# Performance work log

Hardware: AMD Instinct MI355X
Metric: run time of the kernel (lower is better)

## Reference

```python
import jax, jax.numpy as jnp
import numpy as np

B, S, D, H = 2, 2048, 1024, 16
DK = D // H


def setup_inputs() -> dict:
    key = jax.random.key(0)
    ks = jax.random.split(key, 8)
    scale = 1.0 / np.sqrt(D)
    inp = {
        "query": jax.random.normal(ks[0], (B, S, D), dtype=jnp.float32),
        "key": jax.random.normal(ks[1], (B, S, D), dtype=jnp.float32),
        "value": jax.random.normal(ks[2], (B, S, D), dtype=jnp.float32),
        # causal mask, broadcastable over batch and heads
        "mask": jnp.tril(jnp.ones((S, S), dtype=jnp.int32))[None, None, :, :],
        "W_q": jax.random.normal(ks[3], (D, D), dtype=jnp.float32) * scale,
        "W_k": jax.random.normal(ks[4], (D, D), dtype=jnp.float32) * scale,
        "W_v": jax.random.normal(ks[5], (D, D), dtype=jnp.float32) * scale,
        "W_o": jax.random.normal(ks[6], (D, D), dtype=jnp.float32) * scale,
    }
    return inp


def _split_heads(t):
    Bb, Ss, _ = t.shape
    return t.reshape(Bb, Ss, H, DK).transpose(0, 2, 1, 3)  # [B,H,S,DK]


def reference(query, key, value, mask, W_q, W_k, W_v, W_o):
    # Linear(d,d,bias=False): y = x @ W^T (torch stores weight as [out,in])
    Q = _split_heads(query @ W_q.T)
    K = _split_heads(key @ W_k.T)
    V = _split_heads(value @ W_v.T)
    scores = jnp.einsum("bhqd,bhkd->bhqk", Q, K) / jnp.sqrt(jnp.float32(DK))
    scores = jnp.where(mask == 0, -jnp.inf, scores)
    weights = jax.nn.softmax(scores, axis=-1)
    weights = jnp.nan_to_num(weights, nan=0.0)  # fully-masked rows -> 0
    # dropout is identity at inference
    x = jnp.einsum("bhqk,bhkd->bhqd", weights, V)
    x = x.transpose(0, 2, 1, 3).reshape(B, S, D)
    return x @ W_o.T
```

## Files before the change

### kernel.cpp

```cpp
#include <hip/hip_runtime.h>
#include <hip/hip_bf16.h>

#define D_MODEL 1024
#define NHEAD   16
#define HDK     64
#define SEQ     2048
#define BATCH   2
#define BS      (BATCH * SEQ)

typedef __attribute__((ext_vector_type(8))) short bf16x8;
typedef __attribute__((ext_vector_type(4))) float f32x4;

__device__ __forceinline__ unsigned short f2bf(float f) {
    unsigned u = __builtin_bit_cast(unsigned, f);
    u += 0x7fffu + ((u >> 16) & 1u);
    return (unsigned short)(u >> 16);
}

__device__ __forceinline__ unsigned pack_hi(float x, float y) {
    return __builtin_amdgcn_perm(__builtin_bit_cast(unsigned, y),
                                 __builtin_bit_cast(unsigned, x), 0x07060302u);
}

typedef const void __attribute__((address_space(1))) gas_void;
typedef void __attribute__((address_space(3))) las_void;

__device__ __forceinline__ void gll16(const void* g, void* l) {
    __builtin_amdgcn_global_load_lds((gas_void*)g, (las_void*)l, 16, 0, 0);
}

__device__ __forceinline__ void cast_body(const float* __restrict__ src,
                                          unsigned short* __restrict__ dst, int i) {
    const float4* p = (const float4*)src + (size_t)i * 2;
    float4 a = p[0], b = p[1];
    ushort4 lo = make_ushort4(f2bf(a.x), f2bf(a.y), f2bf(a.z), f2bf(a.w));
    ushort4 hi = make_ushort4(f2bf(b.x), f2bf(b.y), f2bf(b.z), f2bf(b.w));
    ushort4* q = (ushort4*)dst + (size_t)i * 2;
    q[0] = lo; q[1] = hi;
}

__global__ __launch_bounds__(256)
void cast_act(const float* a, const float* b, const float* c,
              unsigned short* oa, unsigned short* ob, unsigned short* oc, int n8) {
    int i = blockIdx.x * 256 + threadIdx.x;
    if (i >= n8) return;
    const float* s = blockIdx.y == 0 ? a : blockIdx.y == 1 ? b : c;
    unsigned short* d = blockIdx.y == 0 ? oa : blockIdx.y == 1 ? ob : oc;
    cast_body(s, d, i);
}

__global__ __launch_bounds__(256)
void cast_wt(const float* a, const float* b, const float* c, const float* dd,
             unsigned short* oa, unsigned short* ob, unsigned short* oc, unsigned short* od, int n8) {
    int i = blockIdx.x * 256 + threadIdx.x;
    if (i >= n8) return;
    const float* s = blockIdx.y == 0 ? a : blockIdx.y == 1 ? b : blockIdx.y == 2 ? c : dd;
    unsigned short* d = blockIdx.y == 0 ? oa : blockIdx.y == 1 ? ob : blockIdx.y == 2 ? oc : od;
    cast_body(s, d, i);
}

__device__ __forceinline__ void gemm_kloop128(const unsigned short* __restrict__ X,
                                              const unsigned short* __restrict__ W,
                                              unsigned short* As, unsigned short* Bs,
                                              int bm, int bn, f32x4 acc[4][4]) {
    const int t    = threadIdx.x;
    const int w    = t >> 6;
    const int L    = t & 63;
    const int quad = L >> 4;
    const int lm   = L & 15;
    const int r8   = L >> 3;
    const int sl   = L & 7;
    const int xcol = ((sl ^ r8) & 7) * 8;
    const int wr   = (w >> 1) * 64;
    const int wc   = (w & 1) * 64;

    for (int kt = 0; kt < D_MODEL; kt += 64) {
        __syncthreads();
        #pragma unroll
        for (int i = 0; i < 4; ++i) {
            int c = w * 4 + i;
            gll16(X + (size_t)(bm + c * 8 + r8) * D_MODEL + kt + xcol, &As[c * 512]);
        }
        #pragma unroll
        for (int i = 0; i < 4; ++i) {
            int c = w * 4 + i;
            gll16(W + (size_t)(bn + c * 8 + r8) * D_MODEL + kt + xcol, &Bs[c * 512]);
        }
        __syncthreads();

        #pragma unroll
        for (int ch = 0; ch < 2; ++ch) {
            bf16x8 af[4], bfr[4];
            #pragma unroll
            for (int ms = 0; ms < 4; ++ms) {
                int row = wr + ms * 16 + lm;
                af[ms] = *(const bf16x8*)&As[row * 64 + (((ch * 4 + quad) ^ (row & 7)) * 8)];
            }
            #pragma unroll
            for (int ns = 0; ns < 4; ++ns) {
                int row = wc + ns * 16 + lm;
                bfr[ns] = *(const bf16x8*)&Bs[row * 64 + (((ch * 4 + quad) ^ (row & 7)) * 8)];
            }
            #pragma unroll
            for (int ms = 0; ms < 4; ++ms)
                #pragma unroll
                for (int ns = 0; ns < 4; ++ns)
                    acc[ms][ns] = __builtin_amdgcn_mfma_f32_16x16x32_bf16(
                        af[ms], bfr[ns], acc[ms][ns], 0, 0, 0);
        }
    }
}

__device__ __forceinline__ void gemm_kloop64(const unsigned short* __restrict__ X,
                                             const unsigned short* __restrict__ W,
                                             unsigned short* As, unsigned short* Bs,
                                             int bm, int bn, f32x4 acc[2][4]) {
    const int t    = threadIdx.x;
    const int w    = t >> 6;
    const int L    = t & 63;
    const int quad = L >> 4;
    const int lm   = L & 15;
    const int r8   = L >> 3;
    const int sl   = L & 7;
    const int xcol = ((sl ^ r8) & 7) * 8;

    for (int kt = 0; kt < D_MODEL; kt += 64) {
        __syncthreads();
        #pragma unroll
        for (int i = 0; i < 4; ++i) {
            int c = w * 4 + i;
            gll16(X + (size_t)(bm + c * 8 + r8) * D_MODEL + kt + xcol, &As[c * 512]);
        }
        #pragma unroll
        for (int i = 0; i < 2; ++i) {
            int c = w * 2 + i;
            gll16(W + (size_t)(bn + c * 8 + r8) * D_MODEL + kt + xcol, &Bs[c * 512]);
        }
        __syncthreads();

        #pragma unroll
        for (int ch = 0; ch < 2; ++ch) {
            bf16x8 af[2], bfr[4];
            #pragma unroll
            for (int ms = 0; ms < 2; ++ms) {
                int row = w * 32 + ms * 16 + lm;
                af[ms] = *(const bf16x8*)&As[row * 64 + (((ch * 4 + quad) ^ (row & 7)) * 8)];
            }
            #pragma unroll
            for (int ns = 0; ns < 4; ++ns) {
                int row = ns * 16 + lm;
                bfr[ns] = *(const bf16x8*)&Bs[row * 64 + (((ch * 4 + quad) ^ (row & 7)) * 8)];
            }
            #pragma unroll
            for (int ms = 0; ms < 2; ++ms)
                #pragma unroll
                for (int ns = 0; ns < 4; ++ns)
                    acc[ms][ns] = __builtin_amdgcn_mfma_f32_16x16x32_bf16(
                        af[ms], bfr[ns], acc[ms][ns], 0, 0, 0);
        }
    }
}

__global__ __launch_bounds__(256, 3)
void proj_gemm(const unsigned short* __restrict__ qx, const unsigned short* __restrict__ kx,
               const unsigned short* __restrict__ vx, const unsigned short* __restrict__ wq,
               const unsigned short* __restrict__ wk, const unsigned short* __restrict__ wv,
               unsigned short* __restrict__ Qp, unsigned short* __restrict__ Kp,
               unsigned short* __restrict__ VT) {
    __shared__ __align__(16) unsigned short As[128 * 64];
    __shared__ __align__(16) unsigned short Bs[128 * 64];

    const int p = blockIdx.z;
    const unsigned short* X = p == 0 ? qx : p == 1 ? kx : vx;
    const unsigned short* W = p == 0 ? wq : p == 1 ? wk : wv;
    const int bm = blockIdx.y * 128, bn = blockIdx.x * 128;

    f32x4 acc[4][4];
    #pragma unroll
    for (int ms = 0; ms < 4; ++ms)
        #pragma unroll
        for (int ns = 0; ns < 4; ++ns)
            acc[ms][ns] = (f32x4){0.f, 0.f, 0.f, 0.f};

    gemm_kloop128(X, W, As, Bs, bm, bn, acc);

    const int t = threadIdx.x, w = t >> 6, L = t & 63, quad = L >> 4, lm = L & 15;
    const int wr = (w >> 1) * 64, wc = (w & 1) * 64;
    if (p == 2) {
        const int b    = bm >> 11;
        const int s_in = (bm & (SEQ - 1)) + wr;
        #pragma unroll
        for (int ms = 0; ms < 4; ++ms)
            #pragma unroll
            for (int ns = 0; ns < 4; ++ns) {
                int dg = bn + wc + ns * 16 + lm;
                int h  = dg >> 6, d = dg & 63;
                ushort4 pk = make_ushort4(f2bf(acc[ms][ns][0]), f2bf(acc[ms][ns][1]),
                                          f2bf(acc[ms][ns][2]), f2bf(acc[ms][ns][3]));
                *(ushort4*)&VT[((size_t)((b * NHEAD + h) * HDK + d)) * SEQ +
                               s_in + ms * 16 + quad * 4] = pk;
            }
    } else {
        unsigned short* Y = p == 0 ? Qp : Kp;
        const float scl = p == 0 ? 0.125f : 1.0f;
        #pragma unroll
        for (int ms = 0; ms < 4; ++ms)
            #pragma unroll
            for (int ns = 0; ns < 4; ++ns)
                #pragma unroll
                for (int r = 0; r < 4; ++r)
                    Y[(size_t)(bm + wr + ms * 16 + quad * 4 + r) * D_MODEL +
                      bn + wc + ns * 16 + lm] = f2bf(acc[ms][ns][r] * scl);
    }
}

__global__ __launch_bounds__(256)
void out_gemm(const unsigned short* __restrict__ X, const unsigned short* __restrict__ W,
              float* __restrict__ Y) {
    __shared__ __align__(16) unsigned short As[128 * 64];
    __shared__ __align__(16) unsigned short Bs[64 * 64];
    const int bm = blockIdx.y * 128, bn = blockIdx.x * 64;

    f32x4 acc[2][4];
    #pragma unroll
    for (int ms = 0; ms < 2; ++ms)
        #pragma unroll
        for (int ns = 0; ns < 4; ++ns)
            acc[ms][ns] = (f32x4){0.f, 0.f, 0.f, 0.f};

    gemm_kloop64(X, W, As, Bs, bm, bn, acc);

    const int t = threadIdx.x, w = t >> 6, L = t & 63, quad = L >> 4, lm = L & 15;
    #pragma unroll
    for (int ms = 0; ms < 2; ++ms)
        #pragma unroll
        for (int ns = 0; ns < 4; ++ns)
            #pragma unroll
            for (int r = 0; r < 4; ++r)
                Y[(size_t)(bm + w * 32 + ms * 16 + quad * 4 + r) * D_MODEL +
                  bn + ns * 16 + lm] = acc[ms][ns][r];
}

__global__ __launch_bounds__(256, 3)
void attn_mfma(const unsigned short* __restrict__ Q, const unsigned short* __restrict__ K,
               const unsigned short* __restrict__ VT, unsigned short* __restrict__ A) {
    __shared__ __align__(16) unsigned short Ks[2][64 * 72];
    __shared__ __align__(16) unsigned short Vs[2][64 * 72];
    __shared__ __align__(16) unsigned short Ps[4 * 16 * 72];

    const int t    = threadIdx.x;
    const int w    = t >> 6;
    const int L    = t & 63;
    const int quad = L >> 4;
    const int lm   = L & 15;
    const int h    = blockIdx.y;
    const int b    = blockIdx.z;
    const size_t hb  = (size_t)b * SEQ * D_MODEL + h * HDK;
    const size_t vhb = (size_t)(b * NHEAD + h) * HDK;

    const int srow = t >> 2;
    const int sc   = (t & 3) * 16;
    const unsigned short* kp = K + hb + (size_t)srow * D_MODEL + sc;
    const unsigned short* vp = VT + (vhb + srow) * SEQ + sc;
    unsigned short* ps = &Ps[w * 16 * 72];

    for (int half = 0; half < 2; ++half) {
        const int qt   = half ? 31 - (int)blockIdx.x : (int)blockIdx.x;
        const int q0   = qt * 64;
        const int qrow = q0 + w * 16 + lm;

        bf16x8 Qf0, Qf1;
        {
            const unsigned short* qp = Q + hb + (size_t)qrow * D_MODEL + quad * 8;
            Qf0 = *(const bf16x8*)qp;
            Qf1 = *(const bf16x8*)(qp + 32);
        }

        f32x4 Oacc[4];
        #pragma unroll
        for (int nt = 0; nt < 4; ++nt) Oacc[nt] = (f32x4){0.f, 0.f, 0.f, 0.f};
        float m_run = -INFINITY, l_run = 0.f;

        float4 kr0 = *(const float4*)kp;
        float4 kr1 = *(const float4*)(kp + 8);
        float4 vr0 = *(const float4*)vp;
        float4 vr1 = *(const float4*)(vp + 8);
        *(float4*)&Ks[0][srow * 72 + sc]     = kr0;
        *(float4*)&Ks[0][srow * 72 + sc + 8] = kr1;
        *(float4*)&Vs[0][srow * 72 + sc]     = vr0;
        *(float4*)&Vs[0][srow * 72 + sc + 8] = vr1;
        if (qt >= 1) {
            kr0 = *(const float4*)(kp + (size_t)64 * D_MODEL);
            kr1 = *(const float4*)(kp + (size_t)64 * D_MODEL + 8);
            vr0 = *(const float4*)(vp + 64);
            vr1 = *(const float4*)(vp + 64 + 8);
        }
        __syncthreads();

        int bb = 0;
        for (int kt = 0; kt <= qt; ++kt) {
            const int k0 = kt * 64;
            const unsigned short* Kc = Ks[bb];
            const unsigned short* Vc = Vs[bb];
            if (kt < qt) {
                unsigned short* Kn = Ks[bb ^ 1];
                unsigned short* Vn = Vs[bb ^ 1];
                *(float4*)&Kn[srow * 72 + sc]     = kr0;
                *(float4*)&Kn[srow * 72 + sc + 8] = kr1;
                *(float4*)&Vn[srow * 72 + sc]     = vr0;
                *(float4*)&Vn[srow * 72 + sc + 8] = vr1;
                if (kt + 2 <= qt) {
                    kr0 = *(const float4*)(kp + (size_t)(k0 + 128) * D_MODEL);
                    kr1 = *(const float4*)(kp + (size_t)(k0 + 128) * D_MODEL + 8);
                    vr0 = *(const float4*)(vp + k0 + 128);
                    vr1 = *(const float4*)(vp + k0 + 128 + 8);
                }
            }

            f32x4 S[4];
            #pragma unroll
            for (int ct = 0; ct < 4; ++ct) {
                bf16x8 a0 = *(const bf16x8*)&Kc[(ct * 16 + lm) * 72 + quad * 8];
                bf16x8 a1 = *(const bf16x8*)&Kc[(ct * 16 + lm) * 72 + 32 + quad * 8];
                f32x4 z = (f32x4){0.f, 0.f, 0.f, 0.f};
                z = __builtin_amdgcn_mfma_f32_16x16x32_bf16(a0, Qf0, z, 0, 0, 0);
                z = __builtin_amdgcn_mfma_f32_16x16x32_bf16(a1, Qf1, z, 0, 0, 0);
                S[ct] = z;
            }

            if (k0 + 63 > q0 + w * 16) {
                #pragma unroll
                for (int ct = 0; ct < 4; ++ct)
                    #pragma unroll
                    for (int r = 0; r < 4; ++r)
                        if ((k0 + ct * 16 + quad * 4 + r) > qrow)
                            S[ct][r] = -1e30f;
            }

            float m = fmaxf(fmaxf(fmaxf(S[0][0], S[0][1]), fmaxf(S[0][2], S[0][3])),
                            fmaxf(fmaxf(S[1][0], S[1][1]), fmaxf(S[1][2], S[1][3])));
            m = fmaxf(m, fmaxf(fmaxf(fmaxf(S[2][0], S[2][1]), fmaxf(S[2][2], S[2][3])),
                               fmaxf(fmaxf(S[3][0], S[3][1]), fmaxf(S[3][2], S[3][3]))));
            m = fmaxf(m, __shfl_xor(m, 16));
            m = fmaxf(m, __shfl_xor(m, 32));
            const float m_new = fmaxf(m_run, m);
            const float alpha = __expf(m_run - m_new);
            m_run = m_new;
            float psum = 0.f;
            #pragma unroll
            for (int ct = 0; ct < 4; ++ct)
                #pragma unroll
                for (int r = 0; r < 4; ++r) {
                    float e = __expf(S[ct][r] - m_new);
                    S[ct][r] = e;
                    psum += e;
                }
            psum += __shfl_xor(psum, 16);
            psum += __shfl_xor(psum, 32);
            l_run = l_run * alpha + psum;

            #pragma unroll
            for (int ct = 0; ct < 4; ++ct) {
                uint2 pw = make_uint2(pack_hi(S[ct][0], S[ct][1]),
                                      pack_hi(S[ct][2], S[ct][3]));
                *(uint2*)&ps[lm * 72 + ct * 16 + quad * 4] = pw;
            }
            bf16x8 Pb0 = *(const bf16x8*)&ps[lm * 72 + quad * 8];
            bf16x8 Pb1 = *(const bf16x8*)&ps[lm * 72 + 32 + quad * 8];

            #pragma unroll
            for (int nt = 0; nt < 4; ++nt) {
                bf16x8 a0 = *(const bf16x8*)&Vc[(nt * 16 + lm) * 72 + quad * 8];
                bf16x8 a1 = *(const bf16x8*)&Vc[(nt * 16 + lm) * 72 + 32 + quad * 8];
                f32x4 o = Oacc[nt];
                #pragma unroll
                for (int r = 0; r < 4; ++r) o[r] *= alpha;
                o = __builtin_amdgcn_mfma_f32_16x16x32_bf16(a0, Pb0, o, 0, 0, 0);
                o = __builtin_amdgcn_mfma_f32_16x16x32_bf16(a1, Pb1, o, 0, 0, 0);
                Oacc[nt] = o;
            }

            __syncthreads();
            bb ^= 1;
        }

        const float inv_l = 1.f / l_run;
        #pragma unroll
        for (int nt = 0; nt < 4; ++nt) {
            ushort4 pk = make_ushort4(f2bf(Oacc[nt][0] * inv_l), f2bf(Oacc[nt][1] * inv_l),
                                      f2bf(Oacc[nt][2] * inv_l), f2bf(Oacc[nt][3] * inv_l));
            *(ushort4*)&ps[lm * 72 + nt * 16 + quad * 4] = pk;
        }
        #pragma unroll
        for (int p = 0; p < 2; ++p) {
            int qr = p * 8 + (L >> 3);
            int dc = (L & 7) * 8;
            uint4 val = *(const uint4*)&ps[qr * 72 + dc];
            *(uint4*)&A[hb + (size_t)(q0 + w * 16 + qr) * D_MODEL + dc] = val;
        }
    }
}

extern "C" void kernel_launch(void* const* d_in, const int* in_sizes, int n_in,
                              void* d_out, int out_size, void* d_ws, size_t ws_size,
                              hipStream_t stream) {
    const float* q  = (const float*)d_in[0];
    const float* k  = (const float*)d_in[1];
    const float* v  = (const float*)d_in[2];
    const float* Wq = (const float*)d_in[4];
    const float* Wk = (const float*)d_in[5];
    const float* Wv = (const float*)d_in[6];
    const float* Wo = (const float*)d_in[7];
    float* out = (float*)d_out;

    char* ws = (char*)d_ws;
    const size_t MB = 1024 * 1024;
    unsigned short* qb  = (unsigned short*)(ws + 0 * MB);
    unsigned short* kb  = (unsigned short*)(ws + 8 * MB);
    unsigned short* vb  = (unsigned short*)(ws + 16 * MB);
    unsigned short* wqb = (unsigned short*)(ws + 24 * MB);
    unsigned short* wkb = (unsigned short*)(ws + 26 * MB);
    unsigned short* wvb = (unsigned short*)(ws + 28 * MB);
    unsigned short* wob = (unsigned short*)(ws + 30 * MB);
    unsigned short* Qp  = (unsigned short*)(ws + 32 * MB);
    unsigned short* Kp  = (unsigned short*)(ws + 40 * MB);
    unsigned short* VTp = (unsigned short*)(ws + 48 * MB);
    unsigned short* Ap  = (unsigned short*)(ws + 56 * MB);

    const int nX8 = BS * D_MODEL / 8;
    const int nW8 = D_MODEL * D_MODEL / 8;
    cast_act<<<dim3(nX8 / 256, 3), 256, 0, stream>>>(q, k, v, qb, kb, vb, nX8);
    cast_wt <<<dim3(nW8 / 256, 4), 256, 0, stream>>>(Wq, Wk, Wv, Wo, wqb, wkb, wvb, wob, nW8);

    proj_gemm<<<dim3(D_MODEL / 128, BS / 128, 3), 256, 0, stream>>>(
        qb, kb, vb, wqb, wkb, wvb, Qp, Kp, VTp);

    attn_mfma<<<dim3(16, NHEAD, BATCH), 256, 0, stream>>>(Qp, Kp, VTp, Ap);

    out_gemm<<<dim3(D_MODEL / 64, BS / 128), 256, 0, stream>>>(Ap, wob, out);
}
```

Baseline: 225.9 us.

## Restructure attention: 2 waves × 32 query rows, async LDS loads, XOR-swizzled tiles

The attention kernel now runs 128-thread blocks in which each wave handles two 16-row query slices. K and V fragments are loaded from LDS once per tile and reused across both slices. Global-to-LDS copies use direct async loads (gll16) into XOR-swizzled unpadded tiles in place of staged register copies. The grid is flattened with a remapped block index that groups heads, and the causal mask is applied only on the diagonal tile. The intent is to halve the LDS fragment traffic per query row and overlap loads with compute, at the cost of more registers per wave and fewer waves per block.

```diff
diff --git a/kernel.cpp b/kernel.cpp
--- a/kernel.cpp
+++ b/kernel.cpp
@@ -241,162 +241,173 @@
                   bn + ns * 16 + lm] = acc[ms][ns][r];
 }
 
-__global__ __launch_bounds__(256, 3)
+__global__ __launch_bounds__(128)
 void attn_mfma(const unsigned short* __restrict__ Q, const unsigned short* __restrict__ K,
                const unsigned short* __restrict__ VT, unsigned short* __restrict__ A) {
-    __shared__ __align__(16) unsigned short Ks[2][64 * 72];
-    __shared__ __align__(16) unsigned short Vs[2][64 * 72];
-    __shared__ __align__(16) unsigned short Ps[4 * 16 * 72];
+    __shared__ __align__(16) unsigned short Ks[2][64 * 64];
+    __shared__ __align__(16) unsigned short Vs[2][64 * 64];
+    __shared__ __align__(16) unsigned short Qs[64 * 64];
+    __shared__ __align__(16) unsigned short Ps[2][16 * 68];
 
     const int t    = threadIdx.x;
     const int w    = t >> 6;
     const int L    = t & 63;
     const int quad = L >> 4;
     const int lm   = L & 15;
-    const int h    = blockIdx.y;
-    const int b    = blockIdx.z;
+    const int r8   = L >> 3;
+    const int xcol = ((L & 7) ^ r8) * 8;
+
+    const int f    = blockIdx.x;
+    const int g    = (f & 7) + ((f >> 7) << 3);
+    const int pidx = (f >> 3) & 15;
+    const int b    = g >> 4, h = g & 15;
     const size_t hb  = (size_t)b * SEQ * D_MODEL + h * HDK;
     const size_t vhb = (size_t)(b * NHEAD + h) * HDK;
 
-    const int srow = t >> 2;
-    const int sc   = (t & 3) * 16;
-    const unsigned short* kp = K + hb + (size_t)srow * D_MODEL + sc;
-    const unsigned short* vp = VT + (vhb + srow) * SEQ + sc;
-    unsigned short* ps = &Ps[w * 16 * 72];
+    unsigned short* ps = &Ps[w][0];
 
     for (int half = 0; half < 2; ++half) {
-        const int qt   = half ? 31 - (int)blockIdx.x : (int)blockIdx.x;
-        const int q0   = qt * 64;
-        const int qrow = q0 + w * 16 + lm;
-
-        bf16x8 Qf0, Qf1;
-        {
-            const unsigned short* qp = Q + hb + (size_t)qrow * D_MODEL + quad * 8;
-            Qf0 = *(const bf16x8*)qp;
-            Qf1 = *(const bf16x8*)(qp + 32);
-        }
-
-        f32x4 Oacc[4];
-        #pragma unroll
-        for (int nt = 0; nt < 4; ++nt) Oacc[nt] = (f32x4){0.f, 0.f, 0.f, 0.f};
-        float m_run = -INFINITY, l_run = 0.f;
-
-        float4 kr0 = *(const float4*)kp;
-        float4 kr1 = *(const float4*)(kp + 8);
-        float4 vr0 = *(const float4*)vp;
-        float4 vr1 = *(const float4*)(vp + 8);
-        *(float4*)&Ks[0][srow * 72 + sc]     = kr0;
-        *(float4*)&Ks[0][srow * 72 + sc + 8] = kr1;
-        *(float4*)&Vs[0][srow * 72 + sc]     = vr0;
-        *(float4*)&Vs[0][srow * 72 + sc + 8] = vr1;
-        if (qt >= 1) {
-            kr0 = *(const float4*)(kp + (size_t)64 * D_MODEL);
-            kr1 = *(const float4*)(kp + (size_t)64 * D_MODEL + 8);
-            vr0 = *(const float4*)(vp + 64);
-            vr1 = *(const float4*)(vp + 64 + 8);
+        const int qt = half ? 31 - pidx : pidx;
+        const int q0 = qt * 64;
+
+        #pragma unroll
+        for (int i = 0; i < 4; ++i) {
+            int c = w * 4 + i;
+            gll16(Q + hb + (size_t)(q0 + c * 8 + r8) * D_MODEL + xcol, &Qs[c * 512]);
+            gll16(K + hb + (size_t)(c * 8 + r8) * D_MODEL + xcol, &Ks[0][c * 512]);
+            gll16(VT + (vhb + c * 8 + r8) * SEQ + xcol, &Vs[0][c * 512]);
         }
         __syncthreads();
+
+        bf16x8 Qf[2][2];
+        #pragma unroll
+        for (int s = 0; s < 2; ++s) {
+            int row = w * 32 + s * 16 + lm;
+            Qf[s][0] = *(const bf16x8*)&Qs[row * 64 + ((quad ^ (row & 7)) * 8)];
+            Qf[s][1] = *(const bf16x8*)&Qs[row * 64 + (((4 + quad) ^ (row & 7)) * 8)];
+        }
+
+        f32x4 Oacc[2][4];
+        #pragma unroll
+        for (int s = 0; s < 2; ++s)
+            #pragma unroll
+            for (int nt = 0; nt < 4; ++nt)
+                Oacc[s][nt] = (f32x4){0.f, 0.f, 0.f, 0.f};
+        float m_run[2] = {-INFINITY, -INFINITY};
+        float l_run[2] = {0.f, 0.f};
 
         int bb = 0;
         for (int kt = 0; kt <= qt; ++kt) {
-            const int k0 = kt * 64;
+            if (kt < qt) {
+                #pragma unroll
+                for (int i = 0; i < 4; ++i) {
+                    int c = w * 4 + i;
+                    gll16(K + hb + (size_t)((kt + 1) * 64 + c * 8 + r8) * D_MODEL + xcol,
+                          &Ks[bb ^ 1][c * 512]);
+                    gll16(VT + (vhb + c * 8 + r8) * SEQ + (kt + 1) * 64 + xcol,
+                          &Vs[bb ^ 1][c * 512]);
+                }
+            }
             const unsigned short* Kc = Ks[bb];
             const unsigned short* Vc = Vs[bb];
-            if (kt < qt) {
-                unsigned short* Kn = Ks[bb ^ 1];
-                unsigned short* Vn = Vs[bb ^ 1];
-                *(float4*)&Kn[srow * 72 + sc]     = kr0;
-                *(float4*)&Kn[srow * 72 + sc + 8] = kr1;
-                *(float4*)&Vn[srow * 72 + sc]     = vr0;
-                *(float4*)&Vn[srow * 72 + sc + 8] = vr1;
-                if (kt + 2 <= qt) {
-                    kr0 = *(const float4*)(kp + (size_t)(k0 + 128) * D_MODEL);
-                    kr1 = *(const float4*)(kp + (size_t)(k0 + 128) * D_MODEL + 8);
-                    vr0 = *(const float4*)(vp + k0 + 128);
-                    vr1 = *(const float4*)(vp + k0 + 128 + 8);
+
+            bf16x8 Kf[4][2], Vf[4][2];
+            #pragma unroll
+            for (int ct = 0; ct < 4; ++ct) {
+                int row = ct * 16 + lm;
+                int o0  = row * 64 + ((quad ^ (row & 7)) * 8);
+                int o1  = row * 64 + (((4 + quad) ^ (row & 7)) * 8);
+                Kf[ct][0] = *(const bf16x8*)&Kc[o0];
+                Kf[ct][1] = *(const bf16x8*)&Kc[o1];
+                Vf[ct][0] = *(const bf16x8*)&Vc[o0];
+                Vf[ct][1] = *(const bf16x8*)&Vc[o1];
+            }
+
+            #pragma unroll
+            for (int s = 0; s < 2; ++s) {
+                const int qrow = q0 + w * 32 + s * 16 + lm;
+                f32x4 S[4];
+                #pragma unroll
+                for (int ct = 0; ct < 4; ++ct) {
+                    f32x4 z = (f32x4){0.f, 0.f, 0.f, 0.f};
+                    z = __builtin_amdgcn_mfma_f32_16x16x32_bf16(Kf[ct][0], Qf[s][0], z, 0, 0, 0);
+                    z = __builtin_amdgcn_mfma_f32_16x16x32_bf16(Kf[ct][1], Qf[s][1], z, 0, 0, 0);
+                    S[ct] = z;
                 }
-            }
-
-            f32x4 S[4];
-            #pragma unroll
-            for (int ct = 0; ct < 4; ++ct) {
-                bf16x8 a0 = *(const bf16x8*)&Kc[(ct * 16 + lm) * 72 + quad * 8];
-                bf16x8 a1 = *(const bf16x8*)&Kc[(ct * 16 + lm) * 72 + 32 + quad * 8];
-                f32x4 z = (f32x4){0.f, 0.f, 0.f, 0.f};
-                z = __builtin_amdgcn_mfma_f32_16x16x32_bf16(a0, Qf0, z, 0, 0, 0);
-                z = __builtin_amdgcn_mfma_f32_16x16x32_bf16(a1, Qf1, z, 0, 0, 0);
-                S[ct] = z;
-            }
-
-            if (k0 + 63 > q0 + w * 16) {
+
+                if (kt == qt) {
+                    #pragma unroll
+                    for (int ct = 0; ct < 4; ++ct)
+                        #pragma unroll
+                        for (int r = 0; r < 4; ++r)
+                            if ((q0 + ct * 16 + quad * 4 + r) > qrow)
+                                S[ct][r] = -1e30f;
+                }
+
+                float m = fmaxf(fmaxf(fmaxf(S[0][0], S[0][1]), fmaxf(S[0][2], S[0][3])),
+                                fmaxf(fmaxf(S[1][0], S[1][1]), fmaxf(S[1][2], S[1][3])));
+                m = fmaxf(m, fmaxf(fmaxf(fmaxf(S[2][0], S[2][1]), fmaxf(S[2][2], S[2][3])),
+                                   fmaxf(fmaxf(S[3][0], S[3][1]), fmaxf(S[3][2], S[3][3]))));
+                m = fmaxf(m, __shfl_xor(m, 16));
+                m = fmaxf(m, __shfl_xor(m, 32));
+                const float m_new = fmaxf(m_run[s], m);
+                const float alpha = __expf(m_run[s] - m_new);
+                m_run[s] = m_new;
+                float psum = 0.f;
                 #pragma unroll
                 for (int ct = 0; ct < 4; ++ct)
                     #pragma unroll
-                    for (int r = 0; r < 4; ++r)
-                        if ((k0 + ct * 16 + quad * 4 + r) > qrow)
-                            S[ct][r] = -1e30f;
-            }
-
-            float m = fmaxf(fmaxf(fmaxf(S[0][0], S[0][1]), fmaxf(S[0][2], S[0][3])),
-                            fmaxf(fmaxf(S[1][0], S[1][1]), fmaxf(S[1][2], S[1][3])));
-            m = fmaxf(m, fmaxf(fmaxf(fmaxf(S[2][0], S[2][1]), fmaxf(S[2][2], S[2][3])),
-                               fmaxf(fmaxf(S[3][0], S[3][1]), fmaxf(S[3][2], S[3][3]))));
-            m = fmaxf(m, __shfl_xor(m, 16));
-            m = fmaxf(m, __shfl_xor(m, 32));
-            const float m_new = fmaxf(m_run, m);
-            const float alpha = __expf(m_run - m_new);
-            m_run = m_new;
-            float psum = 0.f;
-            #pragma unroll
-            for (int ct = 0; ct < 4; ++ct)
-                #pragma unroll
-                for (int r = 0; r < 4; ++r) {
-                    float e = __expf(S[ct][r] - m_new);
-                    S[ct][r] = e;
-                    psum += e;
+                    for (int r = 0; r < 4; ++r) {
+                        float e = __expf(S[ct][r] - m_new);
+                        S[ct][r] = e;
+                        psum += e;
+                    }
+                psum += __shfl_xor(psum, 16);
+                psum += __shfl_xor(psum, 32);
+                l_run[s] = l_run[s] * alpha + psum;
+
+                #pragma unroll
+                for (int ct = 0; ct < 4; ++ct) {
+                    uint2 pw = make_uint2(pack_hi(S[ct][0], S[ct][1]),
+                                          pack_hi(S[ct][2], S[ct][3]));
+                    *(uint2*)&ps[lm * 68 + ct * 16 + quad * 4] = pw;
                 }
-            psum += __shfl_xor(psum, 16);
-            psum += __shfl_xor(psum, 32);
-            l_run = l_run * alpha + psum;
-
-            #pragma unroll
-            for (int ct = 0; ct < 4; ++ct) {
-                uint2 pw = make_uint2(pack_hi(S[ct][0], S[ct][1]),
-                                      pack_hi(S[ct][2], S[ct][3]));
-                *(uint2*)&ps[lm * 72 + ct * 16 + quad * 4] = pw;
-            }
-            bf16x8 Pb0 = *(const bf16x8*)&ps[lm * 72 + quad * 8];
-            bf16x8 Pb1 = *(const bf16x8*)&ps[lm * 72 + 32 + quad * 8];
-
-            #pragma unroll
-            for (int nt = 0; nt < 4; ++nt) {
-                bf16x8 a0 = *(const bf16x8*)&Vc[(nt * 16 + lm) * 72 + quad * 8];
-                bf16x8 a1 = *(const bf16x8*)&Vc[(nt * 16 + lm) * 72 + 32 + quad * 8];
-                f32x4 o = Oacc[nt];
-                #pragma unroll
-                for (int r = 0; r < 4; ++r) o[r] *= alpha;
-                o = __builtin_amdgcn_mfma_f32_16x16x32_bf16(a0, Pb0, o, 0, 0, 0);
-                o = __builtin_amdgcn_mfma_f32_16x16x32_bf16(a1, Pb1, o, 0, 0, 0);
-                Oacc[nt] = o;
+                bf16x8 Pb0 = *(const bf16x8*)&ps[lm * 68 + quad * 8];
+                bf16x8 Pb1 = *(const bf16x8*)&ps[lm * 68 + 32 + quad * 8];
+
+                #pragma unroll
+                for (int nt = 0; nt < 4; ++nt) {
+                    f32x4 o = Oacc[s][nt];
+                    #pragma unroll
+                    for (int r = 0; r < 4; ++r) o[r] *= alpha;
+                    o = __builtin_amdgcn_mfma_f32_16x16x32_bf16(Vf[nt][0], Pb0, o, 0, 0, 0);
+                    o = __builtin_amdgcn_mfma_f32_16x16x32_bf16(Vf[nt][1], Pb1, o, 0, 0, 0);
+                    Oacc[s][nt] = o;
+                }
             }
 
             __syncthreads();
             bb ^= 1;
         }
 
-        const float inv_l = 1.f / l_run;
-        #pragma unroll
-        for (int nt = 0; nt < 4; ++nt) {
-            ushort4 pk = make_ushort4(f2bf(Oacc[nt][0] * inv_l), f2bf(Oacc[nt][1] * inv_l),
-                                      f2bf(Oacc[nt][2] * inv_l), f2bf(Oacc[nt][3] * inv_l));
-            *(ushort4*)&ps[lm * 72 + nt * 16 + quad * 4] = pk;
-        }
-        #pragma unroll
-        for (int p = 0; p < 2; ++p) {
-            int qr = p * 8 + (L >> 3);
-            int dc = (L & 7) * 8;
-            uint4 val = *(const uint4*)&ps[qr * 72 + dc];
-            *(uint4*)&A[hb + (size_t)(q0 + w * 16 + qr) * D_MODEL + dc] = val;
+        #pragma unroll
+        for (int s = 0; s < 2; ++s) {
+            const float inv_l = 1.f / l_run[s];
+            #pragma unroll
+            for (int nt = 0; nt < 4; ++nt) {
+                ushort4 pk = make_ushort4(f2bf(Oacc[s][nt][0] * inv_l),
+                                          f2bf(Oacc[s][nt][1] * inv_l),
+                                          f2bf(Oacc[s][nt][2] * inv_l),
+                                          f2bf(Oacc[s][nt][3] * inv_l));
+                *(ushort4*)&ps[lm * 68 + nt * 16 + quad * 4] = pk;
+            }
+            #pragma unroll
+            for (int cc = 0; cc < 2; ++cc) {
+                int chunk = cc * 64 + L;
+                int row = chunk >> 3, seg = chunk & 7;
+                uint4 val = *(const uint4*)&ps[row * 68 + seg * 8];
+                *(uint4*)&A[hb + (size_t)(q0 + w * 32 + s * 16 + row) * D_MODEL + seg * 8] = val;
+            }
         }
     }
 }
@@ -435,7 +446,7 @@
     proj_gemm<<<dim3(D_MODEL / 128, BS / 128, 3), 256, 0, stream>>>(
         qb, kb, vb, wqb, wkb, wvb, Qp, Kp, VTp);
 
-    attn_mfma<<<dim3(16, NHEAD, BATCH), 256, 0, stream>>>(Qp, Kp, VTp, Ap);
+    attn_mfma<<<dim3(512), 128, 0, stream>>>(Qp, Kp, VTp, Ap);
 
     out_gemm<<<dim3(D_MODEL / 64, BS / 128), 256, 0, stream>>>(Ap, wob, out);
 }
```

After: 242.8 us. 1.07x slower.
